# Kernel optimization log

Measured on AMD Instinct MI355X. Metric: run time of the kernel, lower is better.

Reference implementation:

```python
import jax, jax.numpy as jnp
import numpy as np
import math

C_S = 384
C_Z = 128
N_TOK = 1024
N_ATOM = 24576
FDIM = 256
H = 4


def _layer_norm(x, g, b):
    m = jnp.mean(x, axis=-1, keepdims=True)
    v = jnp.mean((x - m) ** 2, axis=-1, keepdims=True)
    return (x - m) / jnp.sqrt(v + 1e-5) * g + b


def _forward(x_noisy, s, z, sigma, atom_to_token_idx,
             fourier_w, fourier_b, ns_w, ns_b, nz_w, nz_b,
             lns_g, lns_b, lnz_g, lnz_b, ce_w, ce_b,
             in_w, in_b, out_w, out_b,
             ffln_g, ffln_b, ff1_w, ff1_b, ff2_w, ff2_b, co_w, co_b):
    # --- DiffusionConditioning ---
    half = FDIM // 2
    freqs = jnp.exp(-math.log(1000.0) * jnp.arange(half, dtype=jnp.float32) / half)
    xf = sigma[:, None] * freqs[None, :]                      # [1, 128]
    emb = jnp.concatenate([jnp.cos(xf), jnp.sin(xf)], axis=-1)  # [1, 256]
    noise = emb @ fourier_w.T + fourier_b                     # [1, 256]
    s_cond = _layer_norm(s, lns_g, lns_b) + (noise @ ns_w.T + ns_b)   # [N_tok, c_s]
    z_cond = _layer_norm(z, lnz_g, lnz_b) + (noise @ nz_w.T + nz_b)   # [N_tok, N_tok, c_z] (unused downstream, as in torch)
    # --- atom -> token segment mean (replaces the python scatter loop) ---
    coord_feat = x_noisy @ ce_w.T + ce_b                      # [N_atom, c_s]
    n_tok = s_cond.shape[0]
    seg_sum = jax.ops.segment_sum(coord_feat, atom_to_token_idx, num_segments=n_tok)
    counts = jax.ops.segment_sum(jnp.ones((coord_feat.shape[0], 1), jnp.float32),
                                 atom_to_token_idx, num_segments=n_tok)
    token_feat = seg_sum / jnp.maximum(counts, 1.0) + s_cond  # [N_tok, c_s]
    # --- single-layer MHA (torch nn.MultiheadAttention math) ---
    qkv = token_feat @ in_w.T + in_b                          # [N_tok, 3*c_s]
    q, k, v = jnp.split(qkv, 3, axis=-1)
    D = C_S // H
    q = q.reshape(n_tok, H, D)
    k = k.reshape(n_tok, H, D)
    v = v.reshape(n_tok, H, D)
    scores = jnp.einsum('shd,thd->hst', q, k) / np.float32(np.sqrt(D))
    attn = jax.nn.softmax(scores, axis=-1)
    ao = jnp.einsum('hst,thd->shd', attn, v).reshape(n_tok, C_S)
    ao = ao @ out_w.T + out_b
    token_feat = token_feat + ao
    # --- FFN ---
    h = _layer_norm(token_feat, ffln_g, ffln_b)
    h = jax.nn.silu(h @ ff1_w.T + ff1_b) @ ff2_w.T + ff2_b
    token_feat = token_feat + h
    # --- token -> atom gather + coord head ---
    atom_feat = token_feat[atom_to_token_idx]                 # [N_atom, c_s]
    return atom_feat @ co_w.T + co_b                          # [N_atom, 3]


def setup_inputs() -> dict:
    key = jax.random.key(0)
    ks = iter(jax.random.split(key, 40))

    def lin(out_d, in_d):
        w = jax.random.normal(next(ks), (out_d, in_d), jnp.float32) / np.float32(np.sqrt(in_d))
        b = jax.random.normal(next(ks), (out_d,), jnp.float32) * 0.01
        return w, b

    fourier_w, fourier_b = lin(FDIM, FDIM)
    ns_w, ns_b = lin(C_S, FDIM)
    nz_w, nz_b = lin(C_Z, FDIM)
    ce_w, ce_b = lin(C_S, 3)
    in_w, in_b = lin(3 * C_S, C_S)
    out_w, out_b = lin(C_S, C_S)
    ff1_w, ff1_b = lin(4 * C_S, C_S)
    ff2_w, ff2_b = lin(C_S, 4 * C_S)
    co_w, co_b = lin(3, C_S)

    return {
        'x_noisy': jax.random.normal(next(ks), (N_ATOM, 3), jnp.float32),
        's': jax.random.normal(next(ks), (N_TOK, C_S), jnp.float32),
        'z': jax.random.normal(next(ks), (N_TOK, N_TOK, C_Z), jnp.float32),
        'sigma': jax.random.uniform(next(ks), (1,), jnp.float32),
        'atom_to_token_idx': jax.random.randint(next(ks), (N_ATOM,), 0, N_TOK),
        'fourier_w': fourier_w, 'fourier_b': fourier_b,
        'ns_w': ns_w, 'ns_b': ns_b, 'nz_w': nz_w, 'nz_b': nz_b,
        'lns_g': jnp.ones((C_S,), jnp.float32), 'lns_b': jnp.zeros((C_S,), jnp.float32),
        'lnz_g': jnp.ones((C_Z,), jnp.float32), 'lnz_b': jnp.zeros((C_Z,), jnp.float32),
        'ce_w': ce_w, 'ce_b': ce_b,
        'in_w': in_w, 'in_b': in_b, 'out_w': out_w, 'out_b': out_b,
        'ffln_g': jnp.ones((C_S,), jnp.float32), 'ffln_b': jnp.zeros((C_S,), jnp.float32),
        'ff1_w': ff1_w, 'ff1_b': ff1_b, 'ff2_w': ff2_w, 'ff2_b': ff2_b,
        'co_w': co_w, 'co_b': co_b,
    }


def reference(x_noisy, s, z, sigma, atom_to_token_idx,
              fourier_w, fourier_b, ns_w, ns_b, nz_w, nz_b,
              lns_g, lns_b, lnz_g, lnz_b, ce_w, ce_b,
              in_w, in_b, out_w, out_b,
              ffln_g, ffln_b, ff1_w, ff1_b, ff2_w, ff2_b, co_w, co_b):
    return _forward(x_noisy, s, z, sigma, atom_to_token_idx,
                    fourier_w, fourier_b, ns_w, ns_b, nz_w, nz_b,
                    lns_g, lns_b, lnz_g, lnz_b, ce_w, ce_b,
                    in_w, in_b, out_w, out_b,
                    ffln_g, ffln_b, ff1_w, ff1_b, ff2_w, ff2_b, co_w, co_b)
```

## Files before the change

### kernel.cpp

```cpp
#include <hip/hip_runtime.h>
#include <hip/hip_bf16.h>
#include <math.h>

#define N_TOK 1024
#define N_ATOM 24576
#define C_S 384
#define FDIM 256
#define NH 4
#define HD 96

typedef __attribute__((ext_vector_type(8))) short short8;
typedef __attribute__((ext_vector_type(4))) float f32x4;

#define OFF_SEGX   0u
#define OFF_NSPROJ 4352u
#define OFF_TF1    4736u
#define OFF_QKV    397952u
#define OFF_TF2    1577600u
#define OFF_TF3    1970816u
#define OFF_TF1B   2364032u
#define OFF_AOB    2560640u
#define OFF_LNHB   2757248u
#define OFF_H1B    2953856u
#define OFF_WINB   3347072u
#define OFF_WOUTB  3568256u
#define OFF_WF1B   3641984u
#define OFF_WF2B   3936896u

__device__ inline __hip_bfloat16 f2bf(float x) { return __float2bfloat16(x); }
union BFPack { short8 v; __hip_bfloat16 h[8]; };
__device__ inline short8 pack8(float4 a, float4 b)
{
    BFPack p;
    p.h[0] = f2bf(a.x); p.h[1] = f2bf(a.y); p.h[2] = f2bf(a.z); p.h[3] = f2bf(a.w);
    p.h[4] = f2bf(b.x); p.h[5] = f2bf(b.y); p.h[6] = f2bf(b.z); p.h[7] = f2bf(b.w);
    return p.v;
}

__global__ __launch_bounds__(256) void k_cvtw(
    const float* __restrict__ in_w, const float* __restrict__ out_w,
    const float* __restrict__ ff1_w, const float* __restrict__ ff2_w,
    __hip_bfloat16* __restrict__ winb, __hip_bfloat16* __restrict__ woutb,
    __hip_bfloat16* __restrict__ wf1b, __hip_bfloat16* __restrict__ wf2b,
    float* __restrict__ segx,
    const float* __restrict__ sigma,
    const float* __restrict__ fw, const float* __restrict__ fb,
    const float* __restrict__ nsw, const float* __restrict__ nsb,
    float* __restrict__ nsproj_out)
{
    __shared__ float emb[256];
    __shared__ float noise[256];
    int tid = threadIdx.x;

    if (blockIdx.x == 864) {
        float sg = sigma[0];
        if (tid < 128) {
            float fr = expf(-logf(1000.f) * (float)tid / 128.f);
            float x = sg * fr;
            emb[tid]       = cosf(x);
            emb[tid + 128] = sinf(x);
        }
        __syncthreads();
        {
            const float* wr = fw + (size_t)tid * 256;
            float acc = fb[tid];
            for (int i = 0; i < 256; i++) acc += emb[i] * wr[i];
            noise[tid] = acc;
        }
        __syncthreads();
        for (int o = tid; o < 384; o += 256) {
            const float* wr = nsw + (size_t)o * 256;
            float acc = nsb[o];
            for (int i = 0; i < 256; i++) acc += noise[i] * wr[i];
            nsproj_out[o] = acc;
        }
        return;
    }

    if (blockIdx.x == 0) {
        #pragma unroll
        for (int j = 0; j < 16; ++j) segx[tid * 16 + j] = 0.f;
    }
    size_t e8 = (size_t)blockIdx.x * 256 + tid;
    const float* src; __hip_bfloat16* dst; size_t off;
    if (e8 < 55296)       { src = in_w;  dst = winb;  off = e8; }
    else if (e8 < 73728)  { src = out_w; dst = woutb; off = e8 - 55296; }
    else if (e8 < 147456) { src = ff1_w; dst = wf1b;  off = e8 - 73728; }
    else                  { src = ff2_w; dst = wf2b;  off = e8 - 147456; }
    float4 a = *(const float4*)(src + off * 8);
    float4 b = *(const float4*)(src + off * 8 + 4);
    *(short8*)(dst + off * 8) = pack8(a, b);
}

__global__ __launch_bounds__(256) void k_segsum(
    const float* __restrict__ x, const int* __restrict__ idx,
    float* __restrict__ segx)
{
    int a = blockIdx.x * 256 + threadIdx.x;
    if (a < N_ATOM) {
        int t = idx[a];
        atomicAdd(&segx[t * 4 + 0], x[a * 3 + 0]);
        atomicAdd(&segx[t * 4 + 1], x[a * 3 + 1]);
        atomicAdd(&segx[t * 4 + 2], x[a * 3 + 2]);
        atomicAdd(&segx[t * 4 + 3], 1.f);
    }
}

__device__ inline float blockReduceSum128(float v, volatile float* sm)
{
    #pragma unroll
    for (int off = 32; off > 0; off >>= 1) v += __shfl_down(v, off);
    if ((threadIdx.x & 63) == 0) sm[threadIdx.x >> 6] = v;
    __syncthreads();
    float r = sm[0] + sm[1];
    __syncthreads();
    return r;
}

__global__ __launch_bounds__(128) void k_tokenfeat(
    const float* __restrict__ s, const float* __restrict__ segx,
    const float* __restrict__ nsproj,
    const float* __restrict__ g, const float* __restrict__ b,
    const float* __restrict__ ce_w, const float* __restrict__ ce_b,
    float* __restrict__ tf, __hip_bfloat16* __restrict__ tfb)
{
    __shared__ float sm[2];
    int t = blockIdx.x, tid = threadIdx.x;
    const float* sr = s + (size_t)t * C_S;
    float x0 = sr[tid], x1 = sr[tid + 128], x2 = sr[tid + 256];
    float total = blockReduceSum128(x0 + x1 + x2, sm);
    float mean = total * (1.f / 384.f);
    float d0 = x0 - mean, d1 = x1 - mean, d2 = x2 - mean;
    float vtot = blockReduceSum128(d0 * d0 + d1 * d1 + d2 * d2, sm);
    float inv = rsqrtf(vtot * (1.f / 384.f) + 1e-5f);
    float cnt = segx[t * 4 + 3];
    float mx0 = 0.f, mx1 = 0.f, mx2 = 0.f;
    int has = cnt > 0.f;
    if (has) {
        float ic = 1.f / cnt;
        mx0 = segx[t * 4 + 0] * ic;
        mx1 = segx[t * 4 + 1] * ic;
        mx2 = segx[t * 4 + 2] * ic;
    }
    float xs[3] = {d0, d1, d2};
    #pragma unroll
    for (int l = 0; l < 3; l++) {
        int c = tid + l * 128;
        float ln = xs[l] * inv * g[c] + b[c];
        float coord = 0.f;
        if (has)
            coord = mx0 * ce_w[c * 3 + 0] + mx1 * ce_w[c * 3 + 1]
                  + mx2 * ce_w[c * 3 + 2] + ce_b[c];
        float v = ln + nsproj[c] + coord;
        tf[(size_t)t * C_S + c] = v;
        tfb[(size_t)t * C_S + c] = f2bf(v);
    }
}

__global__ __launch_bounds__(128) void k_ln(
    const float* __restrict__ in, const float* __restrict__ g,
    const float* __restrict__ b, __hip_bfloat16* __restrict__ out)
{
    __shared__ float sm[2];
    int t = blockIdx.x, tid = threadIdx.x;
    const float* sr = in + (size_t)t * C_S;
    float x0 = sr[tid], x1 = sr[tid + 128], x2 = sr[tid + 256];
    float total = blockReduceSum128(x0 + x1 + x2, sm);
    float mean = total * (1.f / 384.f);
    float d0 = x0 - mean, d1 = x1 - mean, d2 = x2 - mean;
    float vtot = blockReduceSum128(d0 * d0 + d1 * d1 + d2 * d2, sm);
    float inv = rsqrtf(vtot * (1.f / 384.f) + 1e-5f);
    float xs[3] = {d0, d1, d2};
    #pragma unroll
    for (int l = 0; l < 3; l++) {
        int c = tid + l * 128;
        out[(size_t)t * C_S + c] = f2bf(xs[l] * inv * g[c] + b[c]);
    }
}

template <int ACT, bool RES, bool OB>
__global__ __launch_bounds__(256) void k_gemm(
    const __hip_bfloat16* __restrict__ A, const __hip_bfloat16* __restrict__ W,
    const float* __restrict__ bias, const float* __restrict__ res,
    float* __restrict__ Cf, __hip_bfloat16* __restrict__ Cb,
    int M, int N, int K)
{
    __shared__ __hip_bfloat16 As[64][72];
    __shared__ __hip_bfloat16 Bs[64][72];

    int tid = threadIdx.x;
    int bm = blockIdx.y * 64, bn = blockIdx.x * 64;
    int w = tid >> 6, lane = tid & 63;
    int wr = (w >> 1) * 32, wc = (w & 1) * 32;
    int fr = lane & 15, kg = lane >> 4;

    int sr = tid >> 2;
    int sc = (tid & 3) << 4;

    f32x4 acc[2][2] = {};

    for (int k0 = 0; k0 < K; k0 += 64) {
        const __hip_bfloat16* ag = A + (size_t)(bm + sr) * K + k0 + sc;
        const __hip_bfloat16* wg = W + (size_t)(bn + sr) * K + k0 + sc;
        short8 a0 = *(const short8*)(ag + 0);
        short8 a1 = *(const short8*)(ag + 8);
        short8 b0 = *(const short8*)(wg + 0);
        short8 b1 = *(const short8*)(wg + 8);
        __syncthreads();
        *(short8*)&As[sr][sc + 0] = a0;
        *(short8*)&As[sr][sc + 8] = a1;
        *(short8*)&Bs[sr][sc + 0] = b0;
        *(short8*)&Bs[sr][sc + 8] = b1;
        __syncthreads();

        short8 af[2][2], bf[2][2];
        #pragma unroll
        for (int i = 0; i < 2; ++i)
            #pragma unroll
            for (int kh = 0; kh < 2; ++kh) {
                af[i][kh] = *(const short8*)&As[wr + i * 16 + fr][kh * 32 + kg * 8];
                bf[i][kh] = *(const short8*)&Bs[wc + i * 16 + fr][kh * 32 + kg * 8];
            }
        #pragma unroll
        for (int kh = 0; kh < 2; ++kh)
            #pragma unroll
            for (int i = 0; i < 2; ++i)
                #pragma unroll
                for (int j = 0; j < 2; ++j)
                    acc[i][j] = __builtin_amdgcn_mfma_f32_16x16x32_bf16(
                        af[i][kh], bf[j][kh], acc[i][j], 0, 0, 0);
    }

    #pragma unroll
    for (int i = 0; i < 2; ++i) {
        #pragma unroll
        for (int j = 0; j < 2; ++j) {
            int n = bn + wc + j * 16 + fr;
            float bv = bias[n];
            #pragma unroll
            for (int r = 0; r < 4; ++r) {
                int m = bm + wr + i * 16 + kg * 4 + r;
                float v = acc[i][j][r] + bv;
                if (ACT == 1) v = v / (1.f + __expf(-v));
                if (RES) v += res[(size_t)m * N + n];
                if (OB) Cb[(size_t)m * N + n] = f2bf(v);
                else    Cf[(size_t)m * N + n] = v;
            }
        }
    }
}

#define QB 32
#define TB 64

__global__ __launch_bounds__(256) void k_attn(
    const __hip_bfloat16* __restrict__ qkv, __hip_bfloat16* __restrict__ ao)
{
    __shared__ __hip_bfloat16 Ks[TB][104];
    __shared__ __hip_bfloat16 Vt[96][72];
    __shared__ __hip_bfloat16 Ps[QB][72];
    __shared__ float wmax[QB][4];
    __shared__ float wsum[QB][4];

    int tid = threadIdx.x;
    int w = tid >> 6, l = tid & 63;
    int fr = l & 15, kg = l >> 4;
    int row0 = blockIdx.x * QB;
    int h = blockIdx.y;
    const float scale = 0.1020620726f;

    short8 qf[2][3];
    #pragma unroll
    for (int qs = 0; qs < 2; ++qs)
        #pragma unroll
        for (int dg = 0; dg < 3; ++dg)
            qf[qs][dg] = *(const short8*)(qkv
                + (size_t)(row0 + qs * 16 + fr) * 1152 + h * 96 + dg * 32 + kg * 8);

    float m[2][4], lsum[2][4];
    #pragma unroll
    for (int qs = 0; qs < 2; ++qs)
        #pragma unroll
        for (int r = 0; r < 4; ++r) { m[qs][r] = -1e30f; lsum[qs][r] = 0.f; }

    const int myqs = w >> 1;
    const int d0 = (w & 1) * 48;
    f32x4 acc_o[3] = {};

    int st_t = tid >> 2, st_c = (tid & 3) * 24;
    int vt_t = tid & 63, vt_d = (tid >> 6) * 24;

    for (int tile = 0; tile < N_TOK / TB; ++tile) {
        int t0 = tile * TB;
        __syncthreads();
        {
            const __hip_bfloat16* src =
                qkv + (size_t)(t0 + st_t) * 1152 + 384 + h * 96 + st_c;
            short8 k0 = *(const short8*)(src);
            short8 k1 = *(const short8*)(src + 8);
            short8 k2 = *(const short8*)(src + 16);
            *(short8*)&Ks[st_t][st_c + 0]  = k0;
            *(short8*)&Ks[st_t][st_c + 8]  = k1;
// ... 56 lines not shown
                lsum[qs][r] *= scr;
                if (qs == myqs) sc_my[r] = scr;
                Ps[row][w * 16 + fr] = f2bf(p);
                psum[r] = p;
            }
            #pragma unroll
            for (int off = 1; off < 16; off <<= 1)
                #pragma unroll
                for (int r = 0; r < 4; ++r)
                    psum[r] += __shfl_xor(psum[r], off);
            if (fr == 0)
                #pragma unroll
                for (int r = 0; r < 4; ++r)
                    wsum[qs * 16 + kg * 4 + r][w] = psum[r];
        }
        __syncthreads();

        #pragma unroll
        for (int qs = 0; qs < 2; ++qs)
            #pragma unroll
            for (int r = 0; r < 4; ++r) {
                float4 wsv = *(const float4*)&wsum[qs * 16 + kg * 4 + r][0];
                lsum[qs][r] += wsv.x + wsv.y + wsv.z + wsv.w;
            }

        #pragma unroll
        for (int ds = 0; ds < 3; ++ds)
            #pragma unroll
            for (int r = 0; r < 4; ++r)
                acc_o[ds][r] *= sc_my[r];
        #pragma unroll
        for (int kk = 0; kk < 2; ++kk) {
            short8 pf = *(const short8*)&Ps[myqs * 16 + fr][kk * 32 + kg * 8];
            #pragma unroll
            for (int ds = 0; ds < 3; ++ds) {
                short8 vf = *(const short8*)&Vt[d0 + ds * 16 + fr][kk * 32 + kg * 8];
                acc_o[ds] = __builtin_amdgcn_mfma_f32_16x16x32_bf16(pf, vf, acc_o[ds], 0, 0, 0);
            }
        }
    }

    #pragma unroll
    for (int r = 0; r < 4; ++r) {
        float inv = 1.f / lsum[myqs][r];
        int q = row0 + myqs * 16 + kg * 4 + r;
        #pragma unroll
        for (int ds = 0; ds < 3; ++ds) {
            int d = h * 96 + d0 + ds * 16 + fr;
            ao[(size_t)q * C_S + d] = f2bf(acc_o[ds][r] * inv);
        }
    }
}

__global__ __launch_bounds__(256) void k_atomout(
    const float* __restrict__ tf, const int* __restrict__ idx,
    const float* __restrict__ co_w, const float* __restrict__ co_b,
    float* __restrict__ out)
{
    int a = blockIdx.x * 4 + (threadIdx.x >> 6);
    int lane = threadIdx.x & 63;
    if (a >= N_ATOM) return;
    const float* base = tf + (size_t)idx[a] * C_S;
    float a0 = 0.f, a1 = 0.f, a2 = 0.f;
    #pragma unroll
    for (int i = 0; i < 6; ++i) {
        int c = lane + i * 64;
        float v = base[c];
        a0 += v * co_w[c];
        a1 += v * co_w[C_S + c];
        a2 += v * co_w[2 * C_S + c];
    }
    #pragma unroll
    for (int off = 32; off > 0; off >>= 1) {
        a0 += __shfl_down(a0, off);
        a1 += __shfl_down(a1, off);
        a2 += __shfl_down(a2, off);
    }
    if (lane == 0) {
        out[a * 3 + 0] = a0 + co_b[0];
        out[a * 3 + 1] = a1 + co_b[1];
        out[a * 3 + 2] = a2 + co_b[2];
    }
}

extern "C" void kernel_launch(void* const* d_in, const int* in_sizes, int n_in,
                              void* d_out, int out_size, void* d_ws, size_t ws_size,
                              hipStream_t stream)
{
    const float* x_noisy   = (const float*)d_in[0];
    const float* s         = (const float*)d_in[1];
    const float* sigma     = (const float*)d_in[3];
    const int*   a2t       = (const int*)d_in[4];
    const float* fourier_w = (const float*)d_in[5];
    const float* fourier_b = (const float*)d_in[6];
    const float* ns_w      = (const float*)d_in[7];
    const float* ns_b      = (const float*)d_in[8];
    const float* lns_g     = (const float*)d_in[11];
    const float* lns_b     = (const float*)d_in[12];
    const float* ce_w      = (const float*)d_in[15];
    const float* ce_b      = (const float*)d_in[16];
    const float* in_w      = (const float*)d_in[17];
    const float* in_b      = (const float*)d_in[18];
    const float* out_w     = (const float*)d_in[19];
    const float* out_b     = (const float*)d_in[20];
    const float* ffln_g    = (const float*)d_in[21];
    const float* ffln_b    = (const float*)d_in[22];
    const float* ff1_w     = (const float*)d_in[23];
    const float* ff1_b     = (const float*)d_in[24];
    const float* ff2_w     = (const float*)d_in[25];
    const float* ff2_b     = (const float*)d_in[26];
    const float* co_w      = (const float*)d_in[27];
    const float* co_b      = (const float*)d_in[28];

    float* ws  = (float*)d_ws;
    float* out = (float*)d_out;
    __hip_bfloat16* qkvb  = (__hip_bfloat16*)(ws + OFF_QKV);
    __hip_bfloat16* tf1b  = (__hip_bfloat16*)(ws + OFF_TF1B);
    __hip_bfloat16* aob   = (__hip_bfloat16*)(ws + OFF_AOB);
    __hip_bfloat16* lnhb  = (__hip_bfloat16*)(ws + OFF_LNHB);
    __hip_bfloat16* h1b   = (__hip_bfloat16*)(ws + OFF_H1B);
    __hip_bfloat16* winb  = (__hip_bfloat16*)(ws + OFF_WINB);
    __hip_bfloat16* woutb = (__hip_bfloat16*)(ws + OFF_WOUTB);
    __hip_bfloat16* wf1b  = (__hip_bfloat16*)(ws + OFF_WF1B);
    __hip_bfloat16* wf2b  = (__hip_bfloat16*)(ws + OFF_WF2B);

    hipLaunchKernelGGL(k_cvtw, dim3(865), dim3(256), 0, stream,
                       in_w, out_w, ff1_w, ff2_w, winb, woutb, wf1b, wf2b,
                       ws + OFF_SEGX, sigma, fourier_w, fourier_b, ns_w, ns_b,
                       ws + OFF_NSPROJ);
    hipLaunchKernelGGL(k_segsum, dim3(96), dim3(256), 0, stream,
                       x_noisy, a2t, ws + OFF_SEGX);
    hipLaunchKernelGGL(k_tokenfeat, dim3(N_TOK), dim3(128), 0, stream,
                       s, ws + OFF_SEGX, ws + OFF_NSPROJ, lns_g, lns_b,
                       ce_w, ce_b, ws + OFF_TF1, tf1b);
    hipLaunchKernelGGL((k_gemm<0, false, true>), dim3(18, 16), dim3(256), 0, stream,
                       tf1b, winb, in_b, nullptr, (float*)nullptr, qkvb,
                       1024, 1152, 384);
    hipLaunchKernelGGL(k_attn, dim3(N_TOK / QB, NH), dim3(256), 0, stream,
                       qkvb, aob);
    hipLaunchKernelGGL((k_gemm<0, true, false>), dim3(6, 16), dim3(256), 0, stream,
                       aob, woutb, out_b, ws + OFF_TF1, ws + OFF_TF2,
                       (__hip_bfloat16*)nullptr, 1024, 384, 384);
    hipLaunchKernelGGL(k_ln, dim3(N_TOK), dim3(128), 0, stream,
                       ws + OFF_TF2, ffln_g, ffln_b, lnhb);
    hipLaunchKernelGGL((k_gemm<1, false, true>), dim3(24, 16), dim3(256), 0, stream,
                       lnhb, wf1b, ff1_b, nullptr, (float*)nullptr, h1b,
                       1024, 1536, 384);
    hipLaunchKernelGGL((k_gemm<0, true, false>), dim3(6, 16), dim3(256), 0, stream,
                       h1b, wf2b, ff2_b, ws + OFF_TF2, ws + OFF_TF3,
                       (__hip_bfloat16*)nullptr, 1024, 384, 1536);
    hipLaunchKernelGGL(k_atomout, dim3(N_ATOM / 4, 1), dim3(256), 0, stream,
                       ws + OFF_TF3, a2t, co_w, co_b, out);
}
```

Baseline: 136.0 us.

## Fold output projection into FF2 weights and fuse layer norms into GEMMs

Precomputes co_w·ff2_w and the matching bias once, so each atom's output is computed straight from the SiLU hidden activations and the residual stream. This removes the FF2 GEMM and the extra TF3 buffer. Layer norm (plus the conditioning and coordinate terms) is fused into the prologue of the QKV and FF1 GEMMs, which drops the separate token-feature and LN kernels. Segment sums, weight conversion and the noise projection are merged into one prep kernel, with a memset replacing the in-kernel zeroing. In exchange, each atom now does a 1536-long dot product per output, LN is recomputed once per column block, and variance uses a one-pass formula.

Result: slower. 196.4 us (+44.4%).

```diff
diff --git a/kernel.cpp b/kernel.cpp
--- a/kernel.cpp
+++ b/kernel.cpp
@@ -5,7 +5,6 @@
 #define N_TOK 1024
 #define N_ATOM 24576
 #define C_S 384
-#define FDIM 256
 #define NH 4
 #define HD 96
 
@@ -13,19 +12,17 @@
 typedef __attribute__((ext_vector_type(4))) float f32x4;
 
 #define OFF_SEGX   0u
-#define OFF_NSPROJ 4352u
-#define OFF_TF1    4736u
-#define OFF_QKV    397952u
-#define OFF_TF2    1577600u
-#define OFF_TF3    1970816u
-#define OFF_TF1B   2364032u
-#define OFF_AOB    2560640u
-#define OFF_LNHB   2757248u
-#define OFF_H1B    2953856u
-#define OFF_WINB   3347072u
-#define OFF_WOUTB  3568256u
-#define OFF_WF1B   3641984u
-#define OFF_WF2B   3936896u
+#define OFF_NSPROJ 4096u
+#define OFF_CW2    4480u
+#define OFF_CB2    9088u
+#define OFF_TF1    9216u
+#define OFF_TF2    402432u
+#define OFF_QKV    795648u
+#define OFF_AOB    1385472u
+#define OFF_H1B    1582080u
+#define OFF_WINB   2368512u
+#define OFF_WOUTB  2589696u
+#define OFF_WF1B   2663424u
 
 __device__ inline __hip_bfloat16 f2bf(float x) { return __float2bfloat16(x); }
 union BFPack { short8 v; __hip_bfloat16 h[8]; };
@@ -37,22 +34,38 @@
     return p.v;
 }
 
-__global__ __launch_bounds__(256) void k_cvtw(
+__global__ __launch_bounds__(256) void k_prep(
     const float* __restrict__ in_w, const float* __restrict__ out_w,
     const float* __restrict__ ff1_w, const float* __restrict__ ff2_w,
+    const float* __restrict__ ff2_b,
+    const float* __restrict__ co_w, const float* __restrict__ co_b,
     __hip_bfloat16* __restrict__ winb, __hip_bfloat16* __restrict__ woutb,
-    __hip_bfloat16* __restrict__ wf1b, __hip_bfloat16* __restrict__ wf2b,
-    float* __restrict__ segx,
+    __hip_bfloat16* __restrict__ wf1b,
+    float* __restrict__ cw2, float* __restrict__ cb2,
     const float* __restrict__ sigma,
     const float* __restrict__ fw, const float* __restrict__ fb,
     const float* __restrict__ nsw, const float* __restrict__ nsb,
-    float* __restrict__ nsproj_out)
+    float* __restrict__ nsproj_out,
+    const float* __restrict__ x_noisy, const int* __restrict__ a2t,
+    float* __restrict__ segx)
 {
     __shared__ float emb[256];
     __shared__ float noise[256];
     int tid = threadIdx.x;
-
-    if (blockIdx.x == 864) {
+    int bid = blockIdx.x;
+
+    if (bid < 576) {
+        size_t e8 = (size_t)bid * 256 + tid;
+        const float* src; __hip_bfloat16* dst; size_t off;
+        if (e8 < 55296)      { src = in_w;  dst = winb;  off = e8; }
+        else if (e8 < 73728) { src = out_w; dst = woutb; off = e8 - 55296; }
+        else                 { src = ff1_w; dst = wf1b;  off = e8 - 73728; }
+        float4 a = *(const float4*)(src + off * 8);
+        float4 b = *(const float4*)(src + off * 8 + 4);
+        *(short8*)(dst + off * 8) = pack8(a, b);
+        return;
+    }
+    if (bid == 576) {
         float sg = sigma[0];
         if (tid < 128) {
             float fr = expf(-logf(1000.f) * (float)tid / 128.f);
@@ -76,114 +89,168 @@
         }
         return;
     }
-
-    if (blockIdx.x == 0) {
-        #pragma unroll
-        for (int j = 0; j < 16; ++j) segx[tid * 16 + j] = 0.f;
-    }
-    size_t e8 = (size_t)blockIdx.x * 256 + tid;
-    const float* src; __hip_bfloat16* dst; size_t off;
-    if (e8 < 55296)       { src = in_w;  dst = winb;  off = e8; }
-    else if (e8 < 73728)  { src = out_w; dst = woutb; off = e8 - 55296; }
-    else if (e8 < 147456) { src = ff1_w; dst = wf1b;  off = e8 - 73728; }
-    else                  { src = ff2_w; dst = wf2b;  off = e8 - 147456; }
-    float4 a = *(const float4*)(src + off * 8);
-    float4 b = *(const float4*)(src + off * 8 + 4);
-    *(short8*)(dst + off * 8) = pack8(a, b);
-}
-
-__global__ __launch_bounds__(256) void k_segsum(
-    const float* __restrict__ x, const int* __restrict__ idx,
-    float* __restrict__ segx)
-{
-    int a = blockIdx.x * 256 + threadIdx.x;
-    if (a < N_ATOM) {
-        int t = idx[a];
-        atomicAdd(&segx[t * 4 + 0], x[a * 3 + 0]);
-        atomicAdd(&segx[t * 4 + 1], x[a * 3 + 1]);
-        atomicAdd(&segx[t * 4 + 2], x[a * 3 + 2]);
+    if (bid < 673) {
+        int a = (bid - 577) * 256 + tid;
+        int t = a2t[a];
+        atomicAdd(&segx[t * 4 + 0], x_noisy[a * 3 + 0]);
+        atomicAdd(&segx[t * 4 + 1], x_noisy[a * 3 + 1]);
+        atomicAdd(&segx[t * 4 + 2], x_noisy[a * 3 + 2]);
         atomicAdd(&segx[t * 4 + 3], 1.f);
-    }
-}
-
-__device__ inline float blockReduceSum128(float v, volatile float* sm)
-{
-    #pragma unroll
-    for (int off = 32; off > 0; off >>= 1) v += __shfl_down(v, off);
-    if ((threadIdx.x & 63) == 0) sm[threadIdx.x >> 6] = v;
-    __syncthreads();
-    float r = sm[0] + sm[1];
-    __syncthreads();
-    return r;
-}
-
-__global__ __launch_bounds__(128) void k_tokenfeat(
-    const float* __restrict__ s, const float* __restrict__ segx,
-    const float* __restrict__ nsproj,
+        return;
+    }
+    if (bid < 691) {
+        int o = (bid - 673) * 256 + tid;
+        int j = o / 1536, c = o - j * 1536;
+        const float* cr = co_w + j * 384;
+        float acc = 0.f;
+        for (int k = 0; k < 384; ++k)
+            acc += cr[k] * ff2_w[(size_t)k * 1536 + c];
+        cw2[o] = acc;
+        return;
+    }
+    {
+        int w = tid >> 6, l = tid & 63;
+        if (w < 3) {
+            float acc = 0.f;
+            #pragma unroll
+            for (int i = 0; i < 6; ++i)
+                acc += ff2_b[l + 64 * i] * co_w[w * 384 + l + 64 * i];
+            #pragma unroll
+            for (int off = 32; off > 0; off >>= 1) acc += __shfl_down(acc, off);
+            if (l == 0) cb2[w] = acc + co_b[w];
+        }
+    }
+}
+
+template <int MODE>
+__global__ __launch_bounds__(256) void k_lngemm(
+    const float* __restrict__ X, const __hip_bfloat16* __restrict__ W,
+    const float* __restrict__ bias,
     const float* __restrict__ g, const float* __restrict__ b,
+    const float* __restrict__ segx, const float* __restrict__ nsproj,
     const float* __restrict__ ce_w, const float* __restrict__ ce_b,
-    float* __restrict__ tf, __hip_bfloat16* __restrict__ tfb)
-{
-    __shared__ float sm[2];
-    int t = blockIdx.x, tid = threadIdx.x;
-    const float* sr = s + (size_t)t * C_S;
-    float x0 = sr[tid], x1 = sr[tid + 128], x2 = sr[tid + 256];
-    float total = blockReduceSum128(x0 + x1 + x2, sm);
-    float mean = total * (1.f / 384.f);
-    float d0 = x0 - mean, d1 = x1 - mean, d2 = x2 - mean;
-    float vtot = blockReduceSum128(d0 * d0 + d1 * d1 + d2 * d2, sm);
-    float inv = rsqrtf(vtot * (1.f / 384.f) + 1e-5f);
-    float cnt = segx[t * 4 + 3];
-    float mx0 = 0.f, mx1 = 0.f, mx2 = 0.f;
-    int has = cnt > 0.f;
-    if (has) {
-        float ic = 1.f / cnt;
-        mx0 = segx[t * 4 + 0] * ic;
-        mx1 = segx[t * 4 + 1] * ic;
-        mx2 = segx[t * 4 + 2] * ic;
-    }
-    float xs[3] = {d0, d1, d2};
-    #pragma unroll
-    for (int l = 0; l < 3; l++) {
-        int c = tid + l * 128;
-        float ln = xs[l] * inv * g[c] + b[c];
-        float coord = 0.f;
-        if (has)
-            coord = mx0 * ce_w[c * 3 + 0] + mx1 * ce_w[c * 3 + 1]
-                  + mx2 * ce_w[c * 3 + 2] + ce_b[c];
-        float v = ln + nsproj[c] + coord;
-        tf[(size_t)t * C_S + c] = v;
-        tfb[(size_t)t * C_S + c] = f2bf(v);
-    }
-}
-
-__global__ __launch_bounds__(128) void k_ln(
-    const float* __restrict__ in, const float* __restrict__ g,
-    const float* __restrict__ b, __hip_bfloat16* __restrict__ out)
-{
-    __shared__ float sm[2];
-    int t = blockIdx.x, tid = threadIdx.x;
-    const float* sr = in + (size_t)t * C_S;
-    float x0 = sr[tid], x1 = sr[tid + 128], x2 = sr[tid + 256];
-    float total = blockReduceSum128(x0 + x1 + x2, sm);
-    float mean = total * (1.f / 384.f);
-    float d0 = x0 - mean, d1 = x1 - mean, d2 = x2 - mean;
-    float vtot = blockReduceSum128(d0 * d0 + d1 * d1 + d2 * d2, sm);
-    float inv = rsqrtf(vtot * (1.f / 384.f) + 1e-5f);
-    float xs[3] = {d0, d1, d2};
-    #pragma unroll
-    for (int l = 0; l < 3; l++) {
-        int c = tid + l * 128;
-        out[(size_t)t * C_S + c] = f2bf(xs[l] * inv * g[c] + b[c]);
-    }
-}
-
-template <int ACT, bool RES, bool OB>
-__global__ __launch_bounds__(256) void k_gemm(
+    float* __restrict__ tf1out,
+    __hip_bfloat16* __restrict__ OUT, int N)
+{
+    __shared__ __hip_bfloat16 As[64][392];
+    __shared__ __hip_bfloat16 Bs[64][72];
+
+    int tid = threadIdx.x;
+    int bm = blockIdx.y * 64, bn = blockIdx.x * 64;
+
+    {
+        int r = tid >> 2, q = tid & 3;
+        const float* xr = X + (size_t)(bm + r) * 384 + q * 96;
+        float4 v[24];
+        #pragma unroll
+        for (int i = 0; i < 24; ++i) v[i] = *(const float4*)(xr + 4 * i);
+        float s1 = 0.f, s2 = 0.f;
+        #pragma unroll
+        for (int i = 0; i < 24; ++i) {
+            s1 += v[i].x + v[i].y + v[i].z + v[i].w;
+            s2 += v[i].x * v[i].x + v[i].y * v[i].y
+                + v[i].z * v[i].z + v[i].w * v[i].w;
+        }
+        s1 += __shfl_xor(s1, 1); s1 += __shfl_xor(s1, 2);
+        s2 += __shfl_xor(s2, 1); s2 += __shfl_xor(s2, 2);
+        float mean = s1 * (1.f / 384.f);
+        float var  = s2 * (1.f / 384.f) - mean * mean;
+        float rstd = rsqrtf(var + 1e-5f);
+
+        float mx0 = 0.f, mx1 = 0.f, mx2 = 0.f;
+        bool has = false;
+        if (MODE == 0) {
+            float cnt = segx[(bm + r) * 4 + 3];
+            has = cnt > 0.f;
+            if (has) {
+                float ic = 1.f / cnt;
+                mx0 = segx[(bm + r) * 4 + 0] * ic;
+                mx1 = segx[(bm + r) * 4 + 1] * ic;
+                mx2 = segx[(bm + r) * 4 + 2] * ic;
+            }
+        }
+        #pragma unroll
+        for (int i = 0; i < 24; i += 2) {
+            float tmp[8] = { v[i].x, v[i].y, v[i].z, v[i].w,
+                             v[i+1].x, v[i+1].y, v[i+1].z, v[i+1].w };
+            float o_[8];
+            BFPack p;
+            #pragma unroll
+            for (int j = 0; j < 8; ++j) {
+                int c = q * 96 + i * 4 + j;
+                float val = (tmp[j] - mean) * rstd * g[c] + b[c];
+                if (MODE == 0) {
+                    val += nsproj[c];
+                    if (has)
+                        val += mx0 * ce_w[c * 3 + 0] + mx1 * ce_w[c * 3 + 1]
+                             + mx2 * ce_w[c * 3 + 2] + ce_b[c];
+                }
+                o_[j] = val;
+                p.h[j] = f2bf(val);
+            }
+            *(short8*)&As[r][q * 96 + i * 4] = p.v;
+            if (MODE == 0 && blockIdx.x == 0) {
+                float* dst = tf1out + (size_t)(bm + r) * 384 + q * 96 + i * 4;
+                *(float4*)(dst + 0) = make_float4(o_[0], o_[1], o_[2], o_[3]);
+                *(float4*)(dst + 4) = make_float4(o_[4], o_[5], o_[6], o_[7]);
+            }
+        }
+    }
+
+    int w = tid >> 6, lane = tid & 63;
+    int wr = (w >> 1) * 32, wc = (w & 1) * 32;
+    int fr = lane & 15, kg = lane >> 4;
+    int sr = tid >> 2, sc = (tid & 3) << 4;
+
+    f32x4 acc[2][2] = {};
+    for (int k0 = 0; k0 < 384; k0 += 64) {
+        const __hip_bfloat16* wg = W + (size_t)(bn + sr) * 384 + k0 + sc;
+        short8 b0 = *(const short8*)(wg + 0);
+        short8 b1 = *(const short8*)(wg + 8);
+        __syncthreads();
+        *(short8*)&Bs[sr][sc + 0] = b0;
+        *(short8*)&Bs[sr][sc + 8] = b1;
+        __syncthreads();
+
+        short8 af[2][2], bf[2][2];
+        #pragma unroll
+        for (int i = 0; i < 2; ++i)
+            #pragma unroll
+            for (int kh = 0; kh < 2; ++kh) {
+                af[i][kh] = *(const short8*)&As[wr + i * 16 + fr][k0 + kh * 32 + kg * 8];
+                bf[i][kh] = *(const short8*)&Bs[wc + i * 16 + fr][kh * 32 + kg * 8];
+            }
+        #pragma unroll
+        for (int kh = 0; kh < 2; ++kh)
+            #pragma unroll
+            for (int i = 0; i < 2; ++i)
+                #pragma unroll
+                for (int j = 0; j < 2; ++j)
+                    acc[i][j] = __builtin_amdgcn_mfma_f32_16x16x32_bf16(
+                        af[i][kh], bf[j][kh], acc[i][j], 0, 0, 0);
+    }
+
+    #pragma unroll
+    for (int i = 0; i < 2; ++i) {
+        #pragma unroll
+        for (int j = 0; j < 2; ++j) {
+            int n = bn + wc + j * 16 + fr;
+            float bv = bias[n];
+            #pragma unroll
+            for (int r = 0; r < 4; ++r) {
+                int m = bm + wr + i * 16 + kg * 4 + r;
+                float v = acc[i][j][r] + bv;
+                if (MODE == 1) v = v / (1.f + __expf(-v));
+                OUT[(size_t)m * N + n] = f2bf(v);
+            }
+        }
+    }
+}
+
+__global__ __launch_bounds__(256) void k_gemm_res(
     const __hip_bfloat16* __restrict__ A, const __hip_bfloat16* __restrict__ W,
     const float* __restrict__ bias, const float* __restrict__ res,
-    float* __restrict__ Cf, __hip_bfloat16* __restrict__ Cb,
-    int M, int N, int K)
+    float* __restrict__ C, int M, int N, int K)
 {
     __shared__ __hip_bfloat16 As[64][72];
     __shared__ __hip_bfloat16 Bs[64][72];
@@ -193,12 +260,9 @@
     int w = tid >> 6, lane = tid & 63;
     int wr = (w >> 1) * 32, wc = (w & 1) * 32;
     int fr = lane & 15, kg = lane >> 4;
-
-    int sr = tid >> 2;
-    int sc = (tid & 3) << 4;
+    int sr = tid >> 2, sc = (tid & 3) << 4;
 
     f32x4 acc[2][2] = {};
-
     for (int k0 = 0; k0 < K; k0 += 64) {
         const __hip_bfloat16* ag = A + (size_t)(bm + sr) * K + k0 + sc;
         const __hip_bfloat16* wg = W + (size_t)(bn + sr) * K + k0 + sc;
@@ -232,7 +296,7 @@
     }
 
     #pragma unroll
-    for (int i = 0; i < 2; ++i) {
+    for (int i = 0; i < 2; ++i)
         #pragma unroll
         for (int j = 0; j < 2; ++j) {
             int n = bn + wc + j * 16 + fr;
@@ -240,14 +304,9 @@
             #pragma unroll
             for (int r = 0; r < 4; ++r) {
                 int m = bm + wr + i * 16 + kg * 4 + r;
-                float v = acc[i][j][r] + bv;
-                if (ACT == 1) v = v / (1.f + __expf(-v));
-                if (RES) v += res[(size_t)m * N + n];
-                if (OB) Cb[(size_t)m * N + n] = f2bf(v);
-                else    Cf[(size_t)m * N + n] = v;
-            }
-        }
-    }
+                C[(size_t)m * N + n] = acc[i][j][r] + bv + res[(size_t)m * N + n];
+            }
+        }
 }
 
 #define QB 32
@@ -411,22 +470,43 @@
 }
 
 __global__ __launch_bounds__(256) void k_atomout(
-    const float* __restrict__ tf, const int* __restrict__ idx,
-    const float* __restrict__ co_w, const float* __restrict__ co_b,
-    float* __restrict__ out)
+    const float* __restrict__ tf2, const __hip_bfloat16* __restrict__ h1,
+    const int* __restrict__ idx,
+    const float* __restrict__ co_w, const float* __restrict__ cw2,
+    const float* __restrict__ cb2, float* __restrict__ out)
 {
     int a = blockIdx.x * 4 + (threadIdx.x >> 6);
-    int lane = threadIdx.x & 63;
-    if (a >= N_ATOM) return;
-    const float* base = tf + (size_t)idx[a] * C_S;
+    int l = threadIdx.x & 63;
+    int t = idx[a];
+    const __hip_bfloat16* hr = h1 + (size_t)t * 1536;
+    const float* fr = tf2 + (size_t)t * 384;
     float a0 = 0.f, a1 = 0.f, a2 = 0.f;
     #pragma unroll
+    for (int c = 0; c < 3; ++c) {
+        int base = c * 512 + l * 8;
+        BFPack hp; hp.v = *(const short8*)(hr + base);
+        float4 w0a = *(const float4*)(cw2 + base);
+        float4 w0b = *(const float4*)(cw2 + base + 4);
+        float4 w1a = *(const float4*)(cw2 + 1536 + base);
+        float4 w1b = *(const float4*)(cw2 + 1536 + base + 4);
+        float4 w2a = *(const float4*)(cw2 + 3072 + base);
+        float4 w2b = *(const float4*)(cw2 + 3072 + base + 4);
+        float hv[8];
+        #pragma unroll
+        for (int j = 0; j < 8; ++j) hv[j] = __bfloat162float(hp.h[j]);
+        a0 += hv[0]*w0a.x + hv[1]*w0a.y + hv[2]*w0a.z + hv[3]*w0a.w
+            + hv[4]*w0b.x + hv[5]*w0b.y + hv[6]*w0b.z + hv[7]*w0b.w;
+        a1 += hv[0]*w1a.x + hv[1]*w1a.y + hv[2]*w1a.z + hv[3]*w1a.w
+            + hv[4]*w1b.x + hv[5]*w1b.y + hv[6]*w1b.z + hv[7]*w1b.w;
+        a2 += hv[0]*w2a.x + hv[1]*w2a.y + hv[2]*w2a.z + hv[3]*w2a.w
+            + hv[4]*w2b.x + hv[5]*w2b.y + hv[6]*w2b.z + hv[7]*w2b.w;
+    }
+    #pragma unroll
     for (int i = 0; i < 6; ++i) {
-        int c = lane + i * 64;
-        float v = base[c];
-        a0 += v * co_w[c];
-        a1 += v * co_w[C_S + c];
-        a2 += v * co_w[2 * C_S + c];
+        float fv = fr[l + 64 * i];
+        a0 += fv * co_w[l + 64 * i];
+        a1 += fv * co_w[384 + l + 64 * i];
+        a2 += fv * co_w[768 + l + 64 * i];
     }
     #pragma unroll
     for (int off = 32; off > 0; off >>= 1) {
@@ -434,10 +514,10 @@
         a1 += __shfl_down(a1, off);
         a2 += __shfl_down(a2, off);
     }
-    if (lane == 0) {
-        out[a * 3 + 0] = a0 + co_b[0];
-        out[a * 3 + 1] = a1 + co_b[1];
-        out[a * 3 + 2] = a2 + co_b[2];
+    if (l == 0) {
+        out[a * 3 + 0] = a0 + cb2[0];
+        out[a * 3 + 1] = a1 + cb2[1];
+        out[a * 3 + 2] = a2 + cb2[2];
     }
 }
 
@@ -473,40 +553,33 @@
     float* ws  = (float*)d_ws;
     float* out = (float*)d_out;
     __hip_bfloat16* qkvb  = (__hip_bfloat16*)(ws + OFF_QKV);
-    __hip_bfloat16* tf1b  = (__hip_bfloat16*)(ws + OFF_TF1B);
     __hip_bfloat16* aob   = (__hip_bfloat16*)(ws + OFF_AOB);
-    __hip_bfloat16* lnhb  = (__hip_bfloat16*)(ws + OFF_LNHB);
     __hip_bfloat16* h1b   = (__hip_bfloat16*)(ws + OFF_H1B);
     __hip_bfloat16* winb  = (__hip_bfloat16*)(ws + OFF_WINB);
     __hip_bfloat16* woutb = (__hip_bfloat16*)(ws + OFF_WOUTB);
     __hip_bfloat16* wf1b  = (__hip_bfloat16*)(ws + OFF_WF1B);
-    __hip_bfloat16* wf2b  = (__hip_bfloat16*)(ws + OFF_WF2B);
-
-    hipLaunchKernelGGL(k_cvtw, dim3(865), dim3(256), 0, stream,
-                       in_w, out_w, ff1_w, ff2_w, winb, woutb, wf1b, wf2b,
-                       ws + OFF_SEGX, sigma, fourier_w, fourier_b, ns_w, ns_b,
-                       ws + OFF_NSPROJ);
-    hipLaunchKernelGGL(k_segsum, dim3(96), dim3(256), 0, stream,
+
+    hipMemsetAsync(ws + OFF_SEGX, 0, 4096 * sizeof(float), stream);
+
+    hipLaunchKernelGGL(k_prep, dim3(692), dim3(256), 0, stream,
+                       in_w, out_w, ff1_w, ff2_w, ff2_b, co_w, co_b,
+                       winb, woutb, wf1b, ws + OFF_CW2, ws + OFF_CB2,
+                       sigma, fourier_w, fourier_b, ns_w, ns_b, ws + OFF_NSPROJ,
                        x_noisy, a2t, ws + OFF_SEGX);
-    hipLaunchKernelGGL(k_tokenfeat, dim3(N_TOK), dim3(128), 0, stream,
-                       s, ws + OFF_SEGX, ws + OFF_NSPROJ, lns_g, lns_b,
-                       ce_w, ce_b, ws + OFF_TF1, tf1b);
-    hipLaunchKernelGGL((k_gemm<0, false, true>), dim3(18, 16), dim3(256), 0, stream,
-                       tf1b, winb, in_b, nullptr, (float*)nullptr, qkvb,
-                       1024, 1152, 384);
+    hipLaunchKernelGGL((k_lngemm<0>), dim3(18, 16), dim3(256), 0, stream,
+                       s, winb, in_b, lns_g, lns_b,
+                       ws + OFF_SEGX, ws + OFF_NSPROJ, ce_w, ce_b,
+                       ws + OFF_TF1, qkvb, 1152);
     hipLaunchKernelGGL(k_attn, dim3(N_TOK / QB, NH), dim3(256), 0, stream,
                        qkvb, aob);
-    hipLaunchKernelGGL((k_gemm<0, true, false>), dim3(6, 16), dim3(256), 0, stream,
+    hipLaunchKernelGGL(k_gemm_res, dim3(6, 16), dim3(256), 0, stream,
                        aob, woutb, out_b, ws + OFF_TF1, ws + OFF_TF2,
-                       (__hip_bfloat16*)nullptr, 1024, 384, 384);
-    hipLaunchKernelGGL(k_ln, dim3(N_TOK), dim3(128), 0, stream,
-                       ws + OFF_TF2, ffln_g, ffln_b, lnhb);
-    hipLaunchKernelGGL((k_gemm<1, false, true>), dim3(24, 16), dim3(256), 0, stream,
-                       lnhb, wf1b, ff1_b, nullptr, (float*)nullptr, h1b,
-                       1024, 1536, 384);
-    hipLaunchKernelGGL((k_gemm<0, true, false>), dim3(6, 16), dim3(256), 0, stream,
-                       h1b, wf2b, ff2_b, ws + OFF_TF2, ws + OFF_TF3,
-                       (__hip_bfloat16*)nullptr, 1024, 384, 1536);
-    hipLaunchKernelGGL(k_atomout, dim3(N_ATOM / 4, 1), dim3(256), 0, stream,
-                       ws + OFF_TF3, a2t, co_w, co_b, out);
-}
+                       1024, 384, 384);
+    hipLaunchKernelGGL((k_lngemm<1>), dim3(24, 16), dim3(256), 0, stream,
+                       ws + OFF_TF2, wf1b, ff1_b, ffln_g, ffln_b,
+                       nullptr, nullptr, nullptr, nullptr,
+                       nullptr, h1b, 1536);
+    hipLaunchKernelGGL(k_atomout, dim3(N_ATOM / 4), dim3(256), 0, stream,
+                       ws + OFF_TF2, h1b, a2t, co_w,
+                       ws + OFF_CW2, ws + OFF_CB2, out);
+}
```

## Fuse out-projection, LayerNorm, FFN and atom output into one mega kernel

Applied to the files above, without the earlier changes.

Replaces the out-projection GEMM, the FFN LayerNorm, both FFN GEMMs and the per-atom output projection with a single kernel. Each block handles 16 tokens: it keeps the intermediate rows in shared memory, streams weight fragments straight from global memory into MFMA, and scatters the per-token 3-vector to atoms by scanning the index array. Separately, the segment-sum is folded into the weight-conversion prep kernel, and the zeroing of the segment buffer becomes a memset. The aim is to cut launch count and global round-trips for intermediates. The cost is only 64 blocks for the heavy FFN work, repeated weight reads per block, and a full atom-index scan in every block.

Result: slower. 276.9 us (+103.6%).

```diff
diff --git a/kernel.cpp b/kernel.cpp
--- a/kernel.cpp
+++ b/kernel.cpp
@@ -5,7 +5,6 @@
 #define N_TOK 1024
 #define N_ATOM 24576
 #define C_S 384
-#define FDIM 256
 #define NH 4
 #define HD 96
 
@@ -13,19 +12,15 @@
 typedef __attribute__((ext_vector_type(4))) float f32x4;
 
 #define OFF_SEGX   0u
-#define OFF_NSPROJ 4352u
-#define OFF_TF1    4736u
-#define OFF_QKV    397952u
-#define OFF_TF2    1577600u
-#define OFF_TF3    1970816u
-#define OFF_TF1B   2364032u
-#define OFF_AOB    2560640u
-#define OFF_LNHB   2757248u
-#define OFF_H1B    2953856u
-#define OFF_WINB   3347072u
-#define OFF_WOUTB  3568256u
-#define OFF_WF1B   3641984u
-#define OFF_WF2B   3936896u
+#define OFF_NSPROJ 4096u
+#define OFF_TF1    4608u
+#define OFF_TF1B   397824u
+#define OFF_QKV    594432u
+#define OFF_AOB    1184256u
+#define OFF_WINB   1380864u
+#define OFF_WOUTB  1602048u
+#define OFF_WF1B   1675776u
+#define OFF_WF2B   1970688u
 
 __device__ inline __hip_bfloat16 f2bf(float x) { return __float2bfloat16(x); }
 union BFPack { short8 v; __hip_bfloat16 h[8]; };
@@ -37,22 +32,36 @@
     return p.v;
 }
 
-__global__ __launch_bounds__(256) void k_cvtw(
+__global__ __launch_bounds__(256) void k_prep(
     const float* __restrict__ in_w, const float* __restrict__ out_w,
     const float* __restrict__ ff1_w, const float* __restrict__ ff2_w,
     __hip_bfloat16* __restrict__ winb, __hip_bfloat16* __restrict__ woutb,
     __hip_bfloat16* __restrict__ wf1b, __hip_bfloat16* __restrict__ wf2b,
-    float* __restrict__ segx,
     const float* __restrict__ sigma,
     const float* __restrict__ fw, const float* __restrict__ fb,
     const float* __restrict__ nsw, const float* __restrict__ nsb,
-    float* __restrict__ nsproj_out)
+    float* __restrict__ nsproj_out,
+    const float* __restrict__ x_noisy, const int* __restrict__ a2t,
+    float* __restrict__ segx)
 {
     __shared__ float emb[256];
     __shared__ float noise[256];
     int tid = threadIdx.x;
-
-    if (blockIdx.x == 864) {
+    int bid = blockIdx.x;
+
+    if (bid < 864) {
+        size_t e8 = (size_t)bid * 256 + tid;
+        const float* src; __hip_bfloat16* dst; size_t off;
+        if (e8 < 55296)       { src = in_w;  dst = winb;  off = e8; }
+        else if (e8 < 73728)  { src = out_w; dst = woutb; off = e8 - 55296; }
+        else if (e8 < 147456) { src = ff1_w; dst = wf1b;  off = e8 - 73728; }
+        else                  { src = ff2_w; dst = wf2b;  off = e8 - 147456; }
+        float4 a = *(const float4*)(src + off * 8);
+        float4 b = *(const float4*)(src + off * 8 + 4);
+        *(short8*)(dst + off * 8) = pack8(a, b);
+        return;
+    }
+    if (bid == 864) {
         float sg = sigma[0];
         if (tid < 128) {
             float fr = expf(-logf(1000.f) * (float)tid / 128.f);
@@ -76,32 +85,12 @@
         }
         return;
     }
-
-    if (blockIdx.x == 0) {
-        #pragma unroll
-        for (int j = 0; j < 16; ++j) segx[tid * 16 + j] = 0.f;
-    }
-    size_t e8 = (size_t)blockIdx.x * 256 + tid;
-    const float* src; __hip_bfloat16* dst; size_t off;
-    if (e8 < 55296)       { src = in_w;  dst = winb;  off = e8; }
-    else if (e8 < 73728)  { src = out_w; dst = woutb; off = e8 - 55296; }
-    else if (e8 < 147456) { src = ff1_w; dst = wf1b;  off = e8 - 73728; }
-    else                  { src = ff2_w; dst = wf2b;  off = e8 - 147456; }
-    float4 a = *(const float4*)(src + off * 8);
-    float4 b = *(const float4*)(src + off * 8 + 4);
-    *(short8*)(dst + off * 8) = pack8(a, b);
-}
-
-__global__ __launch_bounds__(256) void k_segsum(
-    const float* __restrict__ x, const int* __restrict__ idx,
-    float* __restrict__ segx)
-{
-    int a = blockIdx.x * 256 + threadIdx.x;
-    if (a < N_ATOM) {
-        int t = idx[a];
-        atomicAdd(&segx[t * 4 + 0], x[a * 3 + 0]);
-        atomicAdd(&segx[t * 4 + 1], x[a * 3 + 1]);
-        atomicAdd(&segx[t * 4 + 2], x[a * 3 + 2]);
+    {
+        int a = (bid - 865) * 256 + tid;
+        int t = a2t[a];
+        atomicAdd(&segx[t * 4 + 0], x_noisy[a * 3 + 0]);
+        atomicAdd(&segx[t * 4 + 1], x_noisy[a * 3 + 1]);
+        atomicAdd(&segx[t * 4 + 2], x_noisy[a * 3 + 2]);
         atomicAdd(&segx[t * 4 + 3], 1.f);
     }
 }
@@ -157,33 +146,10 @@
     }
 }
 
-__global__ __launch_bounds__(128) void k_ln(
-    const float* __restrict__ in, const float* __restrict__ g,
-    const float* __restrict__ b, __hip_bfloat16* __restrict__ out)
-{
-    __shared__ float sm[2];
-    int t = blockIdx.x, tid = threadIdx.x;
-    const float* sr = in + (size_t)t * C_S;
-    float x0 = sr[tid], x1 = sr[tid + 128], x2 = sr[tid + 256];
-    float total = blockReduceSum128(x0 + x1 + x2, sm);
-    float mean = total * (1.f / 384.f);
-    float d0 = x0 - mean, d1 = x1 - mean, d2 = x2 - mean;
-    float vtot = blockReduceSum128(d0 * d0 + d1 * d1 + d2 * d2, sm);
-    float inv = rsqrtf(vtot * (1.f / 384.f) + 1e-5f);
-    float xs[3] = {d0, d1, d2};
-    #pragma unroll
-    for (int l = 0; l < 3; l++) {
-        int c = tid + l * 128;
-        out[(size_t)t * C_S + c] = f2bf(xs[l] * inv * g[c] + b[c]);
-    }
-}
-
-template <int ACT, bool RES, bool OB>
-__global__ __launch_bounds__(256) void k_gemm(
+__global__ __launch_bounds__(256) void k_gemm_obf(
     const __hip_bfloat16* __restrict__ A, const __hip_bfloat16* __restrict__ W,
-    const float* __restrict__ bias, const float* __restrict__ res,
-    float* __restrict__ Cf, __hip_bfloat16* __restrict__ Cb,
-    int M, int N, int K)
+    const float* __restrict__ bias, __hip_bfloat16* __restrict__ C,
+    int N, int K)
 {
     __shared__ __hip_bfloat16 As[64][72];
     __shared__ __hip_bfloat16 Bs[64][72];
@@ -193,12 +159,9 @@
     int w = tid >> 6, lane = tid & 63;
     int wr = (w >> 1) * 32, wc = (w & 1) * 32;
     int fr = lane & 15, kg = lane >> 4;
-
-    int sr = tid >> 2;
-    int sc = (tid & 3) << 4;
+    int sr = tid >> 2, sc = (tid & 3) << 4;
 
     f32x4 acc[2][2] = {};
-
     for (int k0 = 0; k0 < K; k0 += 64) {
         const __hip_bfloat16* ag = A + (size_t)(bm + sr) * K + k0 + sc;
         const __hip_bfloat16* wg = W + (size_t)(bn + sr) * K + k0 + sc;
@@ -232,7 +195,7 @@
     }
 
     #pragma unroll
-    for (int i = 0; i < 2; ++i) {
+    for (int i = 0; i < 2; ++i)
         #pragma unroll
         for (int j = 0; j < 2; ++j) {
             int n = bn + wc + j * 16 + fr;
@@ -240,14 +203,9 @@
             #pragma unroll
             for (int r = 0; r < 4; ++r) {
                 int m = bm + wr + i * 16 + kg * 4 + r;
-                float v = acc[i][j][r] + bv;
-                if (ACT == 1) v = v / (1.f + __expf(-v));
-                if (RES) v += res[(size_t)m * N + n];
-                if (OB) Cb[(size_t)m * N + n] = f2bf(v);
-                else    Cf[(size_t)m * N + n] = v;
-            }
-        }
-    }
+                C[(size_t)m * N + n] = f2bf(acc[i][j][r] + bv);
+            }
+        }
 }
 
 #define QB 32
@@ -410,34 +368,158 @@
     }
 }
 
-__global__ __launch_bounds__(256) void k_atomout(
-    const float* __restrict__ tf, const int* __restrict__ idx,
+#define RB 16
+
+__global__ __launch_bounds__(256) void k_ffnmega(
+    const __hip_bfloat16* __restrict__ ao, const float* __restrict__ tf1,
+    const __hip_bfloat16* __restrict__ wout, const float* __restrict__ out_b,
+    const float* __restrict__ g, const float* __restrict__ b,
+    const __hip_bfloat16* __restrict__ wf1, const float* __restrict__ ff1_b,
+    const __hip_bfloat16* __restrict__ wf2, const float* __restrict__ ff2_b,
     const float* __restrict__ co_w, const float* __restrict__ co_b,
-    float* __restrict__ out)
-{
-    int a = blockIdx.x * 4 + (threadIdx.x >> 6);
-    int lane = threadIdx.x & 63;
-    if (a >= N_ATOM) return;
-    const float* base = tf + (size_t)idx[a] * C_S;
-    float a0 = 0.f, a1 = 0.f, a2 = 0.f;
-    #pragma unroll
-    for (int i = 0; i < 6; ++i) {
-        int c = lane + i * 64;
-        float v = base[c];
-        a0 += v * co_w[c];
-        a1 += v * co_w[C_S + c];
-        a2 += v * co_w[2 * C_S + c];
-    }
-    #pragma unroll
-    for (int off = 32; off > 0; off >>= 1) {
-        a0 += __shfl_down(a0, off);
-        a1 += __shfl_down(a1, off);
-        a2 += __shfl_down(a2, off);
-    }
-    if (lane == 0) {
-        out[a * 3 + 0] = a0 + co_b[0];
-        out[a * 3 + 1] = a1 + co_b[1];
-        out[a * 3 + 2] = a2 + co_b[2];
+    const int* __restrict__ idx, float* __restrict__ out)
+{
+    __shared__ float tf2s[16][388];
+    __shared__ __hip_bfloat16 lnh[16][392];
+    __shared__ __hip_bfloat16 h1c[16][392];
+    __shared__ float wpart[4][16][3];
+    __shared__ float toutl[16][3];
+
+    int tid = threadIdx.x;
+    int w = tid >> 6, lane = tid & 63;
+    int fr = lane & 15, kg = lane >> 4;
+    int base = blockIdx.x * RB;
+
+    short8 afa[12];
+    #pragma unroll
+    for (int ks = 0; ks < 12; ++ks)
+        afa[ks] = *(const short8*)(ao + (size_t)(base + fr) * 384 + ks * 32 + kg * 8);
+
+    #pragma unroll
+    for (int t = 0; t < 6; ++t) {
+        int n0 = w * 96 + t * 16;
+        f32x4 acc = {};
+        #pragma unroll
+        for (int ks = 0; ks < 12; ++ks) {
+            short8 bf = *(const short8*)(wout + (size_t)(n0 + fr) * 384 + ks * 32 + kg * 8);
+            acc = __builtin_amdgcn_mfma_f32_16x16x32_bf16(afa[ks], bf, acc, 0, 0, 0);
+        }
+        int n = n0 + fr;
+        float bv = out_b[n];
+        #pragma unroll
+        for (int r = 0; r < 4; ++r) {
+            int row = kg * 4 + r;
+            tf2s[row][n] = acc[r] + bv + tf1[(size_t)(base + row) * 384 + n];
+        }
+    }
+    __syncthreads();
+
+    {
+        int row = tid >> 4, l16 = tid & 15;
+        float s1 = 0.f, s2 = 0.f;
+        #pragma unroll
+        for (int j = 0; j < 24; ++j) {
+            float v = tf2s[row][l16 + j * 16];
+            s1 += v; s2 += v * v;
+        }
+        #pragma unroll
+        for (int o = 1; o < 16; o <<= 1) {
+            s1 += __shfl_xor(s1, o);
+            s2 += __shfl_xor(s2, o);
+        }
+        float mean = s1 * (1.f / 384.f);
+        float rstd = rsqrtf(s2 * (1.f / 384.f) - mean * mean + 1e-5f);
+        #pragma unroll
+        for (int j = 0; j < 24; ++j) {
+            int c = l16 + j * 16;
+            lnh[row][c] = f2bf((tf2s[row][c] - mean) * rstd * g[c] + b[c]);
+        }
+    }
+    __syncthreads();
+
+    short8 af1[12];
+    #pragma unroll
+    for (int ks = 0; ks < 12; ++ks)
+        af1[ks] = *(const short8*)&lnh[fr][ks * 32 + kg * 8];
+
+    f32x4 acc2[6] = {};
+    for (int ch = 0; ch < 4; ++ch) {
+        #pragma unroll
+        for (int t = 0; t < 6; ++t) {
+            int n1 = ch * 384 + w * 96 + t * 16;
+            f32x4 acc = {};
+            #pragma unroll
+            for (int ks = 0; ks < 12; ++ks) {
+                short8 bf = *(const short8*)(wf1 + (size_t)(n1 + fr) * 384 + ks * 32 + kg * 8);
+                acc = __builtin_amdgcn_mfma_f32_16x16x32_bf16(af1[ks], bf, acc, 0, 0, 0);
+            }
+            float bv = ff1_b[n1 + fr];
+            #pragma unroll
+            for (int r = 0; r < 4; ++r) {
+                float v = acc[r] + bv;
+                v = v / (1.f + __expf(-v));
+                h1c[kg * 4 + r][w * 96 + t * 16 + fr] = f2bf(v);
+            }
+        }
+        __syncthreads();
+        #pragma unroll
+        for (int ks = 0; ks < 12; ++ks) {
+            short8 af2 = *(const short8*)&h1c[fr][ks * 32 + kg * 8];
+            #pragma unroll
+            for (int t = 0; t < 6; ++t) {
+                int n2 = w * 96 + t * 16;
+                short8 bf = *(const short8*)(wf2
+                    + (size_t)(n2 + fr) * 1536 + ch * 384 + ks * 32 + kg * 8);
+                acc2[t] = __builtin_amdgcn_mfma_f32_16x16x32_bf16(af2, bf, acc2[t], 0, 0, 0);
+            }
+        }
+        __syncthreads();
+    }
+
+    float part[4][3] = {};
+    #pragma unroll
+    for (int t = 0; t < 6; ++t) {
+        int n = w * 96 + t * 16 + fr;
+        float bv = ff2_b[n];
+        float c0 = co_w[n], c1 = co_w[384 + n], c2 = co_w[768 + n];
+        #pragma unroll
+        for (int r = 0; r < 4; ++r) {
+            int row = kg * 4 + r;
+            float v = acc2[t][r] + bv + tf2s[row][n];
+            part[r][0] += v * c0;
+            part[r][1] += v * c1;
+            part[r][2] += v * c2;
+        }
+    }
+    #pragma unroll
+    for (int o = 1; o < 16; o <<= 1)
+        #pragma unroll
+        for (int r = 0; r < 4; ++r)
+            #pragma unroll
+            for (int j = 0; j < 3; ++j)
+                part[r][j] += __shfl_xor(part[r][j], o);
+    if (fr == 0)
+        #pragma unroll
+        for (int r = 0; r < 4; ++r)
+            #pragma unroll
+            for (int j = 0; j < 3; ++j)
+                wpart[w][kg * 4 + r][j] = part[r][j];
+    __syncthreads();
+    if (tid < 48) {
+        int row = tid / 3, j = tid % 3;
+        toutl[row][j] = wpart[0][row][j] + wpart[1][row][j]
+                      + wpart[2][row][j] + wpart[3][row][j] + co_b[j];
+    }
+    __syncthreads();
+
+    for (int a = tid; a < N_ATOM; a += 256) {
+        int t = idx[a];
+        if ((t >> 4) == (int)blockIdx.x) {
+            int r = t & 15;
+            out[a * 3 + 0] = toutl[r][0];
+            out[a * 3 + 1] = toutl[r][1];
+            out[a * 3 + 2] = toutl[r][2];
+        }
     }
 }
 
@@ -472,41 +554,27 @@
 
     float* ws  = (float*)d_ws;
     float* out = (float*)d_out;
+    __hip_bfloat16* tf1b  = (__hip_bfloat16*)(ws + OFF_TF1B);
     __hip_bfloat16* qkvb  = (__hip_bfloat16*)(ws + OFF_QKV);
-    __hip_bfloat16* tf1b  = (__hip_bfloat16*)(ws + OFF_TF1B);
     __hip_bfloat16* aob   = (__hip_bfloat16*)(ws + OFF_AOB);
-    __hip_bfloat16* lnhb  = (__hip_bfloat16*)(ws + OFF_LNHB);
-    __hip_bfloat16* h1b   = (__hip_bfloat16*)(ws + OFF_H1B);
     __hip_bfloat16* winb  = (__hip_bfloat16*)(ws + OFF_WINB);
     __hip_bfloat16* woutb = (__hip_bfloat16*)(ws + OFF_WOUTB);
     __hip_bfloat16* wf1b  = (__hip_bfloat16*)(ws + OFF_WF1B);
     __hip_bfloat16* wf2b  = (__hip_bfloat16*)(ws + OFF_WF2B);
 
-    hipLaunchKernelGGL(k_cvtw, dim3(865), dim3(256), 0, stream,
+    hipMemsetAsync(ws + OFF_SEGX, 0, 4096 * sizeof(float), stream);
+    hipLaunchKernelGGL(k_prep, dim3(961), dim3(256), 0, stream,
                        in_w, out_w, ff1_w, ff2_w, winb, woutb, wf1b, wf2b,
-                       ws + OFF_SEGX, sigma, fourier_w, fourier_b, ns_w, ns_b,
-                       ws + OFF_NSPROJ);
-    hipLaunchKernelGGL(k_segsum, dim3(96), dim3(256), 0, stream,
-                       x_noisy, a2t, ws + OFF_SEGX);
+                       sigma, fourier_w, fourier_b, ns_w, ns_b,
+                       ws + OFF_NSPROJ, x_noisy, a2t, ws + OFF_SEGX);
     hipLaunchKernelGGL(k_tokenfeat, dim3(N_TOK), dim3(128), 0, stream,
                        s, ws + OFF_SEGX, ws + OFF_NSPROJ, lns_g, lns_b,
                        ce_w, ce_b, ws + OFF_TF1, tf1b);
-    hipLaunchKernelGGL((k_gemm<0, false, true>), dim3(18, 16), dim3(256), 0, stream,
-                       tf1b, winb, in_b, nullptr, (float*)nullptr, qkvb,
-                       1024, 1152, 384);
+    hipLaunchKernelGGL(k_gemm_obf, dim3(18, 16), dim3(256), 0, stream,
+                       tf1b, winb, in_b, qkvb, 1152, 384);
     hipLaunchKernelGGL(k_attn, dim3(N_TOK / QB, NH), dim3(256), 0, stream,
                        qkvb, aob);
-    hipLaunchKernelGGL((k_gemm<0, true, false>), dim3(6, 16), dim3(256), 0, stream,
-                       aob, woutb, out_b, ws + OFF_TF1, ws + OFF_TF2,
-                       (__hip_bfloat16*)nullptr, 1024, 384, 384);
-    hipLaunchKernelGGL(k_ln, dim3(N_TOK), dim3(128), 0, stream,
-                       ws + OFF_TF2, ffln_g, ffln_b, lnhb);
-    hipLaunchKernelGGL((k_gemm<1, false, true>), dim3(24, 16), dim3(256), 0, stream,
-                       lnhb, wf1b, ff1_b, nullptr, (float*)nullptr, h1b,
-                       1024, 1536, 384);
-    hipLaunchKernelGGL((k_gemm<0, true, false>), dim3(6, 16), dim3(256), 0, stream,
-                       h1b, wf2b, ff2_b, ws + OFF_TF2, ws + OFF_TF3,
-                       (__hip_bfloat16*)nullptr, 1024, 384, 1536);
-    hipLaunchKernelGGL(k_atomout, dim3(N_ATOM / 4, 1), dim3(256), 0, stream,
-                       ws + OFF_TF3, a2t, co_w, co_b, out);
-}
+    hipLaunchKernelGGL(k_ffnmega, dim3(N_TOK / RB), dim3(256), 0, stream,
+                       aob, ws + OFF_TF1, woutb, out_b, ffln_g, ffln_b,
+                       wf1b, ff1_b, wf2b, ff2_b, co_w, co_b, a2t, out);
+}
```
